# Optimization experiments

Measured on AMD Instinct MI355X. Metric: run time of the kernel, lower is better.

The kernel has to match this reference:

```python
import jax, jax.numpy as jnp
import numpy as np

C = 16  # CHANNELS
SOBEL_X = jnp.array([[-1., 0., 1.], [-2., 0., 2.], [-1., 0., 1.]], dtype=jnp.float32)
SOBEL_Y = SOBEL_X.T


def _depthwise3x3(x, k3):
    # x: [B,C,H,W]; k3: [3,3] kernel applied per-channel (groups=C, padding=1)
    k = jnp.broadcast_to(k3[None, None], (C, 1, 3, 3))
    return jax.lax.conv_general_dilated(x, k, window_strides=(1, 1), padding='SAME',
                                        feature_group_count=C)


def _alive_mask(x):
    # max_pool2d(alpha, k=3, s=1, p=1) > 0.1 on channel 3
    alpha = x[:, 3:4]
    pooled = jax.lax.reduce_window(alpha, -jnp.inf, jax.lax.max,
                                   (1, 1, 3, 3), (1, 1, 1, 1), 'SAME')
    return pooled > 0.1


def setup_inputs() -> dict:
    key = jax.random.key(0)
    k0, k1, k2, k3 = jax.random.split(key, 4)
    B = 1024
    state_grid = jax.random.uniform(k0, (B, C, 32, 32), dtype=jnp.float32)
    rand_mask = jax.random.randint(k1, (B, 1, 32, 32), 0, 2, dtype=jnp.int32)
    # dense_128: Conv2d(48, 128, k=1); torch default kaiming-uniform-ish -> use scaled normal
    w1 = jax.random.normal(k2, (128, 48), dtype=jnp.float32) * (1.0 / np.sqrt(48.0))
    b1 = jnp.zeros((128,), dtype=jnp.float32)
    # dense_16: original zero-init; use small random weights for a non-degenerate baseline
    w2 = jax.random.normal(k3, (16, 128), dtype=jnp.float32) * 0.01
    b2 = jnp.zeros((16,), dtype=jnp.float32)
    return {"state_grid": state_grid, "rand_mask": rand_mask,
            "w1": w1, "b1": b1, "w2": w2, "b2": b2}


def reference(state_grid, rand_mask, w1, b1, w2, b2):
    # perceive: depthwise sobel-x, sobel-y, identity -> concat to 48 channels
    px = _depthwise3x3(state_grid, SOBEL_X)
    py = _depthwise3x3(state_grid, SOBEL_Y)
    perception = jnp.concatenate([px, py, state_grid], axis=1)  # [B,48,32,32]
    # 1x1 conv MLP
    h = jax.nn.relu(jnp.einsum('oc,bchw->bohw', w1, perception) + b1[None, :, None, None])
    dx = jnp.einsum('oc,bchw->bohw', w2, h) + b2[None, :, None, None]  # [B,16,32,32]
    # stochastic update (0/1 mask broadcast over channels)
    x = state_grid + dx * rand_mask.astype(state_grid.dtype)
    # alive masking
    alive = _alive_mask(state_grid) & _alive_mask(x)
    x = x * alive.astype(state_grid.dtype)
    return jnp.clip(x, 0.0, 1.0)
```

## Files before the change

### kernel.cpp

```cpp
#include <hip/hip_runtime.h>
#include <hip/hip_bf16.h>

#define TPB 256

typedef __attribute__((ext_vector_type(8))) short short8v;
typedef __attribute__((ext_vector_type(4))) float f32x4;

__device__ __forceinline__ float bf2f(unsigned int u) {
    return __uint_as_float(u << 16);
}
__device__ __forceinline__ unsigned int packbf(float x, float y) {
    unsigned int r;
    asm("v_cvt_pk_bf16_f32 %0, %1, %2" : "=v"(r) : "v"(x), "v"(y));
    return r;
}
__device__ __forceinline__ short8v pack8(float4 a, float4 bq) {
    union { unsigned int u[4]; short8v s; } c;
    c.u[0] = packbf(a.x, a.y);  c.u[1] = packbf(a.z, a.w);
    c.u[2] = packbf(bq.x, bq.y); c.u[3] = packbf(bq.z, bq.w);
    return c.s;
}

__global__ __launch_bounds__(TPB, 2) void nca_mfma(
    const float* __restrict__ state,
    const int*   __restrict__ rmask,
    const float* __restrict__ w1,
    const float* __restrict__ b1,
    const float* __restrict__ w2,
    const float* __restrict__ b2,
    float* __restrict__ out)
{
    __shared__ __align__(16) unsigned short sSt[16 * 34 * 36];
    __shared__ __align__(16) unsigned short sP [64 * 72];
    __shared__ __align__(16) unsigned short sH [64 * 136];
    __shared__ __align__(16) float          sA [34 * 34];
    __shared__ unsigned char                sPre[1024];

    const int b    = blockIdx.x;
    const int tid  = threadIdx.x;
    const int lane = tid & 63;
    const int wv   = tid >> 6;
    const int lr   = lane & 15;
    const int lg   = lane >> 4;

    short8v w1f[8][2];
    short8v w2f[4];
    float   b1v[8];
    #pragma unroll
    for (int n = 0; n < 8; ++n) {
        const int f = lr * 8 + n;
        #pragma unroll
        for (int kk = 0; kk < 2; ++kk) {
            const int k0 = kk * 32 + lg * 8;
            if (k0 < 48) {
                const float4 x0 = *reinterpret_cast<const float4*>(w1 + f * 48 + k0);
                const float4 x1 = *reinterpret_cast<const float4*>(w1 + f * 48 + k0 + 4);
                w1f[n][kk] = pack8(x0, x1);
            } else {
                short8v z = {0,0,0,0,0,0,0,0};
                w1f[n][kk] = z;
            }
        }
        b1v[n] = b1[f];
    }
    #pragma unroll
    for (int ks = 0; ks < 4; ++ks) {
        const int k0 = ks * 32 + lg * 8;
        const float4 x0 = *reinterpret_cast<const float4*>(w2 + lr * 128 + k0);
        const float4 x1 = *reinterpret_cast<const float4*>(w2 + lr * 128 + k0 + 4);
        w2f[ks] = pack8(x0, x1);
    }
    const float b2v = b2[lr];

    for (int i = tid; i < 16*34*36/2; i += TPB) reinterpret_cast<unsigned int*>(sSt)[i] = 0u;
    for (int i = tid; i < 64*72/2;    i += TPB) reinterpret_cast<unsigned int*>(sP)[i]  = 0u;
    for (int i = tid; i < 34*34;      i += TPB) sA[i] = 0.f;
    __syncthreads();

    const float* gs = state + (size_t)b * 16384;
    #pragma unroll
    for (int k = 0; k < 16; ++k) {
        const int q = tid + k * TPB;
        const float4 v = reinterpret_cast<const float4*>(gs)[q];
        const int c = q >> 8, rem = q & 255;
        const int h = rem >> 3, wg = rem & 7;
        const int eo = c * 1224 + (h + 1) * 36 + (wg * 4 + 2);
        reinterpret_cast<unsigned int*>(&sSt[eo])[0] = packbf(v.x, v.y);
        reinterpret_cast<unsigned int*>(&sSt[eo])[1] = packbf(v.z, v.w);
    }
    __syncthreads();

    for (int p = tid; p < 1024; p += TPB) {
        const int h = p >> 5, w = p & 31;
        const unsigned short* sa = &sSt[3 * 1224 + h * 36 + (w + 1)];
        float m =          bf2f(sa[0]);
        m = fmaxf(m, bf2f(sa[1]));  m = fmaxf(m, bf2f(sa[2]));
        m = fmaxf(m, bf2f(sa[36])); m = fmaxf(m, bf2f(sa[37])); m = fmaxf(m, bf2f(sa[38]));
        m = fmaxf(m, bf2f(sa[72])); m = fmaxf(m, bf2f(sa[73])); m = fmaxf(m, bf2f(sa[74]));
        sPre[p] = (m > 0.1f) ? 1 : 0;
    }

    auto do_gate = [&](int pb, const float* xp) {
        float av = 0.f;
        if (lane < 16) {
            const int p = pb + lane;
            const int h = p >> 5, w = p & 31;
            const float* sa = &sA[h * 34 + w];
            float m =          sa[0];
            m = fmaxf(m, sa[1]);  m = fmaxf(m, sa[2]);
            m = fmaxf(m, sa[34]); m = fmaxf(m, sa[35]); m = fmaxf(m, sa[36]);
            m = fmaxf(m, sa[68]); m = fmaxf(m, sa[69]); m = fmaxf(m, sa[70]);
            av = ((m > 0.1f) && (sPre[p] != 0)) ? 1.f : 0.f;
        }
        const float g0 = __shfl(av, lg * 4 + 0);
        const float g1 = __shfl(av, lg * 4 + 1);
        const float g2 = __shfl(av, lg * 4 + 2);
        const float g3 = __shfl(av, lg * 4 + 3);
        float4 ov;
        ov.x = g0 * fminf(fmaxf(xp[0], 0.f), 1.f);
        ov.y = g1 * fminf(fmaxf(xp[1], 0.f), 1.f);
        ov.z = g2 * fminf(fmaxf(xp[2], 0.f), 1.f);
        ov.w = g3 * fminf(fmaxf(xp[3], 0.f), 1.f);
        *reinterpret_cast<float4*>(&out[(size_t)b * 16384 + lr * 1024 + pb + lg * 4]) = ov;
    };

    float xq[2][4];

    for (int s = 0; s < 16; ++s) {
        const int pbase = s * 64 + wv * 16;
        const int4   mi  = *reinterpret_cast<const int4*>(&rmask[b * 1024 + pbase + lg * 4]);
        const float4 idv = *reinterpret_cast<const float4*>(&state[(size_t)b * 16384 + lr * 1024 + pbase + lg * 4]);

        {
            const int cg   = lane & 7;
            const int pl   = lane >> 3;
            const int c0   = cg * 2;
            const int hloc = wv >> 1;
            const int w0   = (wv & 1) * 16 + pl * 2;
            const int h    = s * 2 + hloc;
            const int j0   = hloc * 32 + w0;
            float sx0[2], sx1[2], sy0[2], sy1[2], id0[2], id1[2];
            #pragma unroll
            for (int ci = 0; ci < 2; ++ci) {
                const unsigned short* bp = &sSt[(c0 + ci) * 1224 + h * 36 + w0];
                float A[3], Bv[3], Cv[3], D[3];
                #pragma unroll
                for (int dr = 0; dr < 3; ++dr) {
                    const unsigned int* rp = reinterpret_cast<const unsigned int*>(bp + dr * 36);
                    const unsigned int u0 = rp[0], u1 = rp[1], u2 = rp[2];
                    A[dr]  = bf2f(u0 >> 16);
                    Bv[dr] = bf2f(u1 & 0xffffu);
                    Cv[dr] = bf2f(u1 >> 16);
                    D[dr]  = bf2f(u2 & 0xffffu);
                }
                const float csa = A[0]  + 2.f * A[1]  + A[2];
                const float csb = Bv[0] + 2.f * Bv[1] + Bv[2];
                const float csc = Cv[0] + 2.f * Cv[1] + Cv[2];
                const float csd = D[0]  + 2.f * D[1]  + D[2];
                sx0[ci] = csc - csa;
                sx1[ci] = csd - csb;
                sy0[ci] = (A[2] + 2.f * Bv[2] + Cv[2]) - (A[0] + 2.f * Bv[0] + Cv[0]);
                sy1[ci] = (Bv[2] + 2.f * Cv[2] + D[2]) - (Bv[0] + 2.f * Cv[0] + D[0]);
                id0[ci] = Bv[1];
                id1[ci] = Cv[1];
            }
            unsigned int* r0 = reinterpret_cast<unsigned int*>(&sP[j0 * 72 + c0]);
            unsigned int* r1 = reinterpret_cast<unsigned int*>(&sP[(j0 + 1) * 72 + c0]);
            r0[0]  = packbf(sx0[0], sx0[1]);
            r0[8]  = packbf(sy0[0], sy0[1]);
            r0[16] = packbf(id0[0], id0[1]);
            r1[0]  = packbf(sx1[0], sx1[1]);
            r1[8]  = packbf(sy1[0], sy1[1]);
            r1[16] = packbf(id1[0], id1[1]);
        }

        f32x4 acc1[8];
        #pragma unroll
        for (int n = 0; n < 8; ++n) { acc1[n][0]=0.f; acc1[n][1]=0.f; acc1[n][2]=0.f; acc1[n][3]=0.f; }
        #pragma unroll
        for (int kk = 0; kk < 2; ++kk) {
            const short8v a = *reinterpret_cast<const short8v*>(&sP[(wv * 16 + lr) * 72 + kk * 32 + lg * 8]);
            #pragma unroll
            for (int n = 0; n < 8; ++n)
                acc1[n] = __builtin_amdgcn_mfma_f32_16x16x32_bf16(a, w1f[n][kk], acc1[n], 0, 0, 0);
        }
        #pragma unroll
        for (int r = 0; r < 4; ++r) {
            const int row = wv * 16 + lg * 4 + r;
            uint4 u;
            u.x = packbf(fmaxf(acc1[0][r] + b1v[0], 0.f), fmaxf(acc1[1][r] + b1v[1], 0.f));
            u.y = packbf(fmaxf(acc1[2][r] + b1v[2], 0.f), fmaxf(acc1[3][r] + b1v[3], 0.f));
            u.z = packbf(fmaxf(acc1[4][r] + b1v[4], 0.f), fmaxf(acc1[5][r] + b1v[5], 0.f));
            u.w = packbf(fmaxf(acc1[6][r] + b1v[6], 0.f), fmaxf(acc1[7][r] + b1v[7], 0.f));
            *reinterpret_cast<uint4*>(&sH[row * 136 + lr * 8]) = u;
        }

        f32x4 acc2; acc2[0]=0.f; acc2[1]=0.f; acc2[2]=0.f; acc2[3]=0.f;
        #pragma unroll
        for (int ksx = 0; ksx < 4; ++ksx) {
            const short8v a2 = *reinterpret_cast<const short8v*>(&sH[(wv * 16 + lr) * 136 + ksx * 32 + lg * 8]);
            acc2 = __builtin_amdgcn_mfma_f32_16x16x32_bf16(a2, w2f[ksx], acc2, 0, 0, 0);
        }
        float xv[4];
        xv[0] = fmaf(acc2[0] + b2v, (float)mi.x, idv.x);
        xv[1] = fmaf(acc2[1] + b2v, (float)mi.y, idv.y);
        xv[2] = fmaf(acc2[2] + b2v, (float)mi.z, idv.z);
        xv[3] = fmaf(acc2[3] + b2v, (float)mi.w, idv.w);
        if (lr == 3) {
            const int p0 = pbase + lg * 4;
            const int h2 = p0 >> 5, w2c = p0 & 31;
            float* dst = &sA[(h2 + 1) * 34 + (w2c + 1)];
            dst[0] = xv[0]; dst[1] = xv[1]; dst[2] = xv[2]; dst[3] = xv[3];
        }

        const int par = s & 1;
        if (s >= 2) do_gate((s - 2) * 64 + wv * 16, xq[par]);
        xq[par][0] = xv[0]; xq[par][1] = xv[1]; xq[par][2] = xv[2]; xq[par][3] = xv[3];

        __syncthreads();
    }
    do_gate(14 * 64 + wv * 16, xq[0]);
    do_gate(15 * 64 + wv * 16, xq[1]);
}

extern "C" void kernel_launch(void* const* d_in, const int* in_sizes, int n_in,
                              void* d_out, int out_size, void* d_ws, size_t ws_size,
                              hipStream_t stream) {
    const float* state = (const float*)d_in[0];
    const int*   rmask = (const int*)d_in[1];
    const float* w1    = (const float*)d_in[2];
    const float* b1    = (const float*)d_in[3];
    const float* w2    = (const float*)d_in[4];
    const float* b2    = (const float*)d_in[5];
    float* outp = (float*)d_out;

    const int B = in_sizes[0] / (16 * 32 * 32);
    hipLaunchKernelGGL(nca_mfma, dim3(B), dim3(TPB), 0, stream,
                       state, rmask, w1, b1, w2, b2, outp);
}
```

Baseline: 190.2 us.

## Stream state rows through ring buffer to cut LDS and raise occupancy

The full 34-row bf16 state halo tile in shared memory is replaced with an 8-row ring buffer. Each iteration prefetches the next rows from global memory and writes them in after compute, and the alive tile shrinks to a 9-row ring as well. The pre-update alive mask is now computed inline from the alpha channel during the Sobel stage instead of in a separate pass. Launch bounds go from 2 to 4 blocks per CU, so more blocks can be resident to hide latency, at the cost of tighter register budgets and more complex ring indexing.

```diff
diff --git a/kernel.cpp b/kernel.cpp
--- a/kernel.cpp
+++ b/kernel.cpp
@@ -21,7 +21,7 @@
     return c.s;
 }
 
-__global__ __launch_bounds__(TPB, 2) void nca_mfma(
+__global__ __launch_bounds__(TPB, 4) void nca_mfma(
     const float* __restrict__ state,
     const int*   __restrict__ rmask,
     const float* __restrict__ w1,
@@ -30,10 +30,10 @@
     const float* __restrict__ b2,
     float* __restrict__ out)
 {
-    __shared__ __align__(16) unsigned short sSt[16 * 34 * 36];
+    __shared__ __align__(16) unsigned short sSt[16 * 8 * 36];
     __shared__ __align__(16) unsigned short sP [64 * 72];
     __shared__ __align__(16) unsigned short sH [64 * 136];
-    __shared__ __align__(16) float          sA [34 * 34];
+    __shared__ __align__(16) float          sA [9 * 34];
     __shared__ unsigned char                sPre[1024];
 
     const int b    = blockIdx.x;
@@ -72,44 +72,41 @@
     }
     const float b2v = b2[lr];
 
-    for (int i = tid; i < 16*34*36/2; i += TPB) reinterpret_cast<unsigned int*>(sSt)[i] = 0u;
-    for (int i = tid; i < 64*72/2;    i += TPB) reinterpret_cast<unsigned int*>(sP)[i]  = 0u;
-    for (int i = tid; i < 34*34;      i += TPB) sA[i] = 0.f;
+    for (int i = tid; i < 16*8*36/2; i += TPB) reinterpret_cast<unsigned int*>(sSt)[i] = 0u;
+    for (int i = tid; i < 64*72/2;   i += TPB) reinterpret_cast<unsigned int*>(sP)[i]  = 0u;
+    for (int i = tid; i < 9*34;      i += TPB) sA[i] = 0.f;
     __syncthreads();
 
     const float* gs = state + (size_t)b * 16384;
     #pragma unroll
-    for (int k = 0; k < 16; ++k) {
+    for (int k = 0; k < 3; ++k) {
         const int q = tid + k * TPB;
-        const float4 v = reinterpret_cast<const float4*>(gs)[q];
-        const int c = q >> 8, rem = q & 255;
-        const int h = rem >> 3, wg = rem & 7;
-        const int eo = c * 1224 + (h + 1) * 36 + (wg * 4 + 2);
-        reinterpret_cast<unsigned int*>(&sSt[eo])[0] = packbf(v.x, v.y);
-        reinterpret_cast<unsigned int*>(&sSt[eo])[1] = packbf(v.z, v.w);
+        if (q < 640) {
+            const int ch = q / 40, rem = q - ch * 40;
+            const int row = rem >> 3, px4 = rem & 7;
+            const float4 v = reinterpret_cast<const float4*>(gs)[ch * 256 + row * 8 + px4];
+            unsigned int* dst = reinterpret_cast<unsigned int*>(&sSt[ch * 288 + row * 36 + px4 * 4 + 2]);
+            dst[0] = packbf(v.x, v.y);
+            dst[1] = packbf(v.z, v.w);
+        }
     }
     __syncthreads();
 
-    for (int p = tid; p < 1024; p += TPB) {
-        const int h = p >> 5, w = p & 31;
-        const unsigned short* sa = &sSt[3 * 1224 + h * 36 + (w + 1)];
-        float m =          bf2f(sa[0]);
-        m = fmaxf(m, bf2f(sa[1]));  m = fmaxf(m, bf2f(sa[2]));
-        m = fmaxf(m, bf2f(sa[36])); m = fmaxf(m, bf2f(sa[37])); m = fmaxf(m, bf2f(sa[38]));
-        m = fmaxf(m, bf2f(sa[72])); m = fmaxf(m, bf2f(sa[73])); m = fmaxf(m, bf2f(sa[74]));
-        sPre[p] = (m > 0.1f) ? 1 : 0;
-    }
-
-    auto do_gate = [&](int pb, const float* xp) {
+    auto do_gate = [&](int g, const float* xp) {
         float av = 0.f;
         if (lane < 16) {
-            const int p = pb + lane;
+            const int p = g * 64 + wv * 16 + lane;
             const int h = p >> 5, w = p & 31;
-            const float* sa = &sA[h * 34 + w];
-            float m =          sa[0];
-            m = fmaxf(m, sa[1]);  m = fmaxf(m, sa[2]);
-            m = fmaxf(m, sa[34]); m = fmaxf(m, sa[35]); m = fmaxf(m, sa[36]);
-            m = fmaxf(m, sa[68]); m = fmaxf(m, sa[69]); m = fmaxf(m, sa[70]);
+            const int sm = (h - 1 >= 0) ? ((h - 1) & 7) : 8;
+            const int s0 = h & 7;
+            const int sp = (h + 1 <= 31) ? ((h + 1) & 7) : 8;
+            const float* r0 = &sA[sm * 34 + w];
+            const float* r1 = &sA[s0 * 34 + w];
+            const float* r2 = &sA[sp * 34 + w];
+            float m =          r0[0];
+            m = fmaxf(m, r0[1]); m = fmaxf(m, r0[2]);
+            m = fmaxf(m, r1[0]); m = fmaxf(m, r1[1]); m = fmaxf(m, r1[2]);
+            m = fmaxf(m, r2[0]); m = fmaxf(m, r2[1]); m = fmaxf(m, r2[2]);
             av = ((m > 0.1f) && (sPre[p] != 0)) ? 1.f : 0.f;
         }
         const float g0 = __shfl(av, lg * 4 + 0);
@@ -121,15 +118,25 @@
         ov.y = g1 * fminf(fmaxf(xp[1], 0.f), 1.f);
         ov.z = g2 * fminf(fmaxf(xp[2], 0.f), 1.f);
         ov.w = g3 * fminf(fmaxf(xp[3], 0.f), 1.f);
-        *reinterpret_cast<float4*>(&out[(size_t)b * 16384 + lr * 1024 + pb + lg * 4]) = ov;
+        *reinterpret_cast<float4*>(&out[(size_t)b * 16384 + lr * 1024 + g * 64 + wv * 16 + lg * 4]) = ov;
     };
 
     float xq[2][4];
+
+    const int pf_ch  = tid >> 4;
+    const int pf_rl  = (tid & 15) >> 3;
+    const int pf_px4 = tid & 7;
 
     for (int s = 0; s < 16; ++s) {
         const int pbase = s * 64 + wv * 16;
         const int4   mi  = *reinterpret_cast<const int4*>(&rmask[b * 1024 + pbase + lg * 4]);
         const float4 idv = *reinterpret_cast<const float4*>(&state[(size_t)b * 16384 + lr * 1024 + pbase + lg * 4]);
+
+        const int pf_row = 2 * s + 5 + pf_rl;
+        float4 pf = {0.f, 0.f, 0.f, 0.f};
+        const bool pf_do = (pf_row <= 32);
+        if (pf_row <= 31)
+            pf = reinterpret_cast<const float4*>(gs)[pf_ch * 256 + pf_row * 8 + pf_px4];
 
         {
             const int cg   = lane & 7;
@@ -137,16 +144,18 @@
             const int c0   = cg * 2;
             const int hloc = wv >> 1;
             const int w0   = (wv & 1) * 16 + pl * 2;
-            const int h    = s * 2 + hloc;
+            const int rr0  = 2 * s + hloc - 1;
             const int j0   = hloc * 32 + w0;
             float sx0[2], sx1[2], sy0[2], sy1[2], id0[2], id1[2];
+            float mp0 = 0.f, mp1 = 0.f;
             #pragma unroll
             for (int ci = 0; ci < 2; ++ci) {
-                const unsigned short* bp = &sSt[(c0 + ci) * 1224 + h * 36 + w0];
+                const unsigned short* bp = &sSt[(c0 + ci) * 288 + w0];
                 float A[3], Bv[3], Cv[3], D[3];
                 #pragma unroll
                 for (int dr = 0; dr < 3; ++dr) {
-                    const unsigned int* rp = reinterpret_cast<const unsigned int*>(bp + dr * 36);
+                    const int slot = ((rr0 + dr) & 7) * 36;
+                    const unsigned int* rp = reinterpret_cast<const unsigned int*>(bp + slot);
                     const unsigned int u0 = rp[0], u1 = rp[1], u2 = rp[2];
                     A[dr]  = bf2f(u0 >> 16);
                     Bv[dr] = bf2f(u1 & 0xffffu);
@@ -163,6 +172,13 @@
                 sy1[ci] = (Bv[2] + 2.f * Cv[2] + D[2]) - (Bv[0] + 2.f * Cv[0] + D[0]);
                 id0[ci] = Bv[1];
                 id1[ci] = Cv[1];
+                if (ci == 1) {
+                    #pragma unroll
+                    for (int dr = 0; dr < 3; ++dr) {
+                        mp0 = fmaxf(mp0, fmaxf(fmaxf(A[dr], Bv[dr]), Cv[dr]));
+                        mp1 = fmaxf(mp1, fmaxf(fmaxf(Bv[dr], Cv[dr]), D[dr]));
+                    }
+                }
             }
             unsigned int* r0 = reinterpret_cast<unsigned int*>(&sP[j0 * 72 + c0]);
             unsigned int* r1 = reinterpret_cast<unsigned int*>(&sP[(j0 + 1) * 72 + c0]);
@@ -172,6 +188,10 @@
             r1[0]  = packbf(sx1[0], sx1[1]);
             r1[8]  = packbf(sy1[0], sy1[1]);
             r1[16] = packbf(id1[0], id1[1]);
+            if (cg == 1) {
+                sPre[s * 64 + j0]     = (mp0 > 0.1f) ? 1 : 0;
+                sPre[s * 64 + j0 + 1] = (mp1 > 0.1f) ? 1 : 0;
+            }
         }
 
         f32x4 acc1[8];
@@ -209,18 +229,25 @@
         if (lr == 3) {
             const int p0 = pbase + lg * 4;
             const int h2 = p0 >> 5, w2c = p0 & 31;
-            float* dst = &sA[(h2 + 1) * 34 + (w2c + 1)];
+            float* dst = &sA[(h2 & 7) * 34 + (w2c + 1)];
             dst[0] = xv[0]; dst[1] = xv[1]; dst[2] = xv[2]; dst[3] = xv[3];
         }
 
         const int par = s & 1;
-        if (s >= 2) do_gate((s - 2) * 64 + wv * 16, xq[par]);
+        if (s >= 2) do_gate(s - 2, xq[par]);
         xq[par][0] = xv[0]; xq[par][1] = xv[1]; xq[par][2] = xv[2]; xq[par][3] = xv[3];
 
+        if (pf_do) {
+            unsigned int* dst = reinterpret_cast<unsigned int*>(
+                &sSt[pf_ch * 288 + (pf_row & 7) * 36 + pf_px4 * 4 + 2]);
+            dst[0] = packbf(pf.x, pf.y);
+            dst[1] = packbf(pf.z, pf.w);
+        }
+
         __syncthreads();
     }
-    do_gate(14 * 64 + wv * 16, xq[0]);
-    do_gate(15 * 64 + wv * 16, xq[1]);
+    do_gate(14, xq[0]);
+    do_gate(15, xq[1]);
 }
 
 extern "C" void kernel_launch(void* const* d_in, const int* in_sizes, int n_in,
```

New measurement: 273.2 us. +43.6%, slower.

## Fold Sobel filters into first-layer weights and run perception as implicit-GEMM conv

Applied to the files above, without the earlier changes.

Premultiplies the w1 weights by the Sobel and identity taps so the 3x3 depthwise perception plus the first 1x1 layer become a single 3x3 convolution done by MFMA over a 144-wide K (9 taps x 16 channels, padded to 5 K-steps). The state is stored channel-last (HWC) in LDS so each MFMA A fragment is a direct 16-byte read of 8 channels at one tap. This removes the scalar Sobel stencil code and the sP staging buffer. In exchange it issues 40 MFMAs per step instead of 16, and it rounds the folded weights to bf16, which changes numerical behaviour slightly.

```diff
diff --git a/kernel.cpp b/kernel.cpp
--- a/kernel.cpp
+++ b/kernel.cpp
@@ -2,6 +2,7 @@
 #include <hip/hip_bf16.h>
 
 #define TPB 256
+#define RS  592
 
 typedef __attribute__((ext_vector_type(8))) short short8v;
 typedef __attribute__((ext_vector_type(4))) float f32x4;
@@ -13,6 +14,12 @@
     unsigned int r;
     asm("v_cvt_pk_bf16_f32 %0, %1, %2" : "=v"(r) : "v"(x), "v"(y));
     return r;
+}
+__device__ __forceinline__ short8v pack8f(const float* v) {
+    union { unsigned int u[4]; short8v s; } c;
+    c.u[0] = packbf(v[0], v[1]); c.u[1] = packbf(v[2], v[3]);
+    c.u[2] = packbf(v[4], v[5]); c.u[3] = packbf(v[6], v[7]);
+    return c.s;
 }
 __device__ __forceinline__ short8v pack8(float4 a, float4 bq) {
     union { unsigned int u[4]; short8v s; } c;
@@ -21,7 +28,7 @@
     return c.s;
 }
 
-__global__ __launch_bounds__(TPB, 2) void nca_mfma(
+__global__ __launch_bounds__(TPB, 2) void nca_conv(
     const float* __restrict__ state,
     const int*   __restrict__ rmask,
     const float* __restrict__ w1,
@@ -30,8 +37,7 @@
     const float* __restrict__ b2,
     float* __restrict__ out)
 {
-    __shared__ __align__(16) unsigned short sSt[16 * 34 * 36];
-    __shared__ __align__(16) unsigned short sP [64 * 72];
+    __shared__ __align__(16) unsigned short sSt[34 * RS];
     __shared__ __align__(16) unsigned short sH [64 * 136];
     __shared__ __align__(16) float          sA [34 * 34];
     __shared__ unsigned char                sPre[1024];
@@ -42,68 +48,101 @@
     const int wv   = tid >> 6;
     const int lr   = lane & 15;
     const int lg   = lane >> 4;
-
-    short8v w1f[8][2];
+    const int lh   = lg >> 1;
+    const int c0   = (lg & 1) * 8;
+
+
+    short8v w1f[8][5];
     short8v w2f[4];
     float   b1v[8];
-    #pragma unroll
-    for (int n = 0; n < 8; ++n) {
-        const int f = lr * 8 + n;
-        #pragma unroll
-        for (int kk = 0; kk < 2; ++kk) {
-            const int k0 = kk * 32 + lg * 8;
-            if (k0 < 48) {
-                const float4 x0 = *reinterpret_cast<const float4*>(w1 + f * 48 + k0);
-                const float4 x1 = *reinterpret_cast<const float4*>(w1 + f * 48 + k0 + 4);
-                w1f[n][kk] = pack8(x0, x1);
-            } else {
-                short8v z = {0,0,0,0,0,0,0,0};
-                w1f[n][kk] = z;
+    {
+        const float SXT[10] = {-1.f,0.f,1.f,-2.f,0.f,2.f,-1.f,0.f,1.f,0.f};
+        const float SYT[10] = {-1.f,-2.f,-1.f,0.f,0.f,0.f,1.f,2.f,1.f,0.f};
+        #pragma unroll
+        for (int n = 0; n < 8; ++n) {
+            const int f = lr * 8 + n;
+            float wx[8], wy[8], ws[8];
+            {
+                const float4 a0 = *reinterpret_cast<const float4*>(w1 + f*48 + c0);
+                const float4 a1 = *reinterpret_cast<const float4*>(w1 + f*48 + c0 + 4);
+                const float4 y0 = *reinterpret_cast<const float4*>(w1 + f*48 + 16 + c0);
+                const float4 y1 = *reinterpret_cast<const float4*>(w1 + f*48 + 16 + c0 + 4);
+                const float4 s0 = *reinterpret_cast<const float4*>(w1 + f*48 + 32 + c0);
+                const float4 s1 = *reinterpret_cast<const float4*>(w1 + f*48 + 32 + c0 + 4);
+                wx[0]=a0.x; wx[1]=a0.y; wx[2]=a0.z; wx[3]=a0.w; wx[4]=a1.x; wx[5]=a1.y; wx[6]=a1.z; wx[7]=a1.w;
+                wy[0]=y0.x; wy[1]=y0.y; wy[2]=y0.z; wy[3]=y0.w; wy[4]=y1.x; wy[5]=y1.y; wy[6]=y1.z; wy[7]=y1.w;
+                ws[0]=s0.x; ws[1]=s0.y; ws[2]=s0.z; ws[3]=s0.w; ws[4]=s1.x; ws[5]=s1.y; ws[6]=s1.z; ws[7]=s1.w;
             }
-        }
-        b1v[n] = b1[f];
-    }
-    #pragma unroll
-    for (int ks = 0; ks < 4; ++ks) {
-        const int k0 = ks * 32 + lg * 8;
-        const float4 x0 = *reinterpret_cast<const float4*>(w2 + lr * 128 + k0);
-        const float4 x1 = *reinterpret_cast<const float4*>(w2 + lr * 128 + k0 + 4);
-        w2f[ks] = pack8(x0, x1);
+            #pragma unroll
+            for (int kk = 0; kk < 5; ++kk) {
+                const float sx = lh ? SXT[2*kk+1] : SXT[2*kk];
+                const float sy = lh ? SYT[2*kk+1] : SYT[2*kk];
+                const float si = (kk == 2 && lh == 0) ? 1.f : 0.f;
+                const float kill = (kk == 4 && lh == 1) ? 0.f : 1.f;
+                float v[8];
+                #pragma unroll
+                for (int e = 0; e < 8; ++e)
+                    v[e] = (wx[e]*sx + wy[e]*sy + ws[e]*si) * kill;
+                w1f[n][kk] = pack8f(v);
+            }
+            b1v[n] = b1[f];
+        }
+        #pragma unroll
+        for (int ks = 0; ks < 4; ++ks) {
+            const int k0 = ks * 32 + lg * 8;
+            const float4 x0 = *reinterpret_cast<const float4*>(w2 + lr*128 + k0);
+            const float4 x1 = *reinterpret_cast<const float4*>(w2 + lr*128 + k0 + 4);
+            w2f[ks] = pack8(x0, x1);
+        }
     }
     const float b2v = b2[lr];
 
-    for (int i = tid; i < 16*34*36/2; i += TPB) reinterpret_cast<unsigned int*>(sSt)[i] = 0u;
-    for (int i = tid; i < 64*72/2;    i += TPB) reinterpret_cast<unsigned int*>(sP)[i]  = 0u;
-    for (int i = tid; i < 34*34;      i += TPB) sA[i] = 0.f;
+    for (int i = tid; i < 34*RS/2; i += TPB) reinterpret_cast<unsigned int*>(sSt)[i] = 0u;
+    for (int i = tid; i < 34*34;   i += TPB) sA[i] = 0.f;
     __syncthreads();
 
     const float* gs = state + (size_t)b * 16384;
     #pragma unroll
-    for (int k = 0; k < 16; ++k) {
-        const int q = tid + k * TPB;
-        const float4 v = reinterpret_cast<const float4*>(gs)[q];
-        const int c = q >> 8, rem = q & 255;
-        const int h = rem >> 3, wg = rem & 7;
-        const int eo = c * 1224 + (h + 1) * 36 + (wg * 4 + 2);
-        reinterpret_cast<unsigned int*>(&sSt[eo])[0] = packbf(v.x, v.y);
-        reinterpret_cast<unsigned int*>(&sSt[eo])[1] = packbf(v.z, v.w);
+    for (int i = 0; i < 8; ++i) {
+        const int q4 = tid + i * TPB;
+        const int cpair = q4 >> 8;
+        const int px4 = q4 & 255;
+        const int h = px4 >> 3, w4 = px4 & 7;
+        const float4 va = reinterpret_cast<const float4*>(gs)[cpair*512 + px4];
+        const float4 vb = reinterpret_cast<const float4*>(gs)[cpair*512 + 256 + px4];
+        unsigned int* dst = reinterpret_cast<unsigned int*>(sSt);
+        const int base = (h + 1) * (RS/2) + (w4*4 + 2) * 8 + cpair;
+        dst[base]      = packbf(va.x, vb.x);
+        dst[base + 8]  = packbf(va.y, vb.y);
+        dst[base + 16] = packbf(va.z, vb.z);
+        dst[base + 24] = packbf(va.w, vb.w);
     }
     __syncthreads();
 
     for (int p = tid; p < 1024; p += TPB) {
         const int h = p >> 5, w = p & 31;
-        const unsigned short* sa = &sSt[3 * 1224 + h * 36 + (w + 1)];
-        float m =          bf2f(sa[0]);
-        m = fmaxf(m, bf2f(sa[1]));  m = fmaxf(m, bf2f(sa[2]));
-        m = fmaxf(m, bf2f(sa[36])); m = fmaxf(m, bf2f(sa[37])); m = fmaxf(m, bf2f(sa[38]));
-        m = fmaxf(m, bf2f(sa[72])); m = fmaxf(m, bf2f(sa[73])); m = fmaxf(m, bf2f(sa[74]));
+        float m = 0.f;
+        #pragma unroll
+        for (int dr = 0; dr < 3; ++dr)
+            #pragma unroll
+            for (int dc = 0; dc < 3; ++dc)
+                m = fmaxf(m, bf2f(sSt[(h+dr)*RS + (w+1+dc)*16 + 3]));
         sPre[p] = (m > 0.1f) ? 1 : 0;
     }
 
-    auto do_gate = [&](int pb, const float* xp) {
+    int roff[5];
+    #pragma unroll
+    for (int kk = 0; kk < 5; ++kk) {
+        const int te = 2*kk, to = (2*kk+1 > 8) ? 8 : 2*kk+1;
+        const int re = (te/3)*RS + (te%3)*16;
+        const int ro = (to/3)*RS + (to%3)*16;
+        roff[kk] = lh ? ro : re;
+    }
+
+    auto do_gate = [&](int g, const float* xp) {
         float av = 0.f;
         if (lane < 16) {
-            const int p = pb + lane;
+            const int p = g * 64 + wv * 16 + lane;
             const int h = p >> 5, w = p & 31;
             const float* sa = &sA[h * 34 + w];
             float m =          sa[0];
@@ -121,7 +160,7 @@
         ov.y = g1 * fminf(fmaxf(xp[1], 0.f), 1.f);
         ov.z = g2 * fminf(fmaxf(xp[2], 0.f), 1.f);
         ov.w = g3 * fminf(fmaxf(xp[3], 0.f), 1.f);
-        *reinterpret_cast<float4*>(&out[(size_t)b * 16384 + lr * 1024 + pb + lg * 4]) = ov;
+        *reinterpret_cast<float4*>(&out[(size_t)b * 16384 + lr * 1024 + g * 64 + wv * 16 + lg * 4]) = ov;
     };
 
     float xq[2][4];
@@ -131,58 +170,24 @@
         const int4   mi  = *reinterpret_cast<const int4*>(&rmask[b * 1024 + pbase + lg * 4]);
         const float4 idv = *reinterpret_cast<const float4*>(&state[(size_t)b * 16384 + lr * 1024 + pbase + lg * 4]);
 
-        {
-            const int cg   = lane & 7;
-            const int pl   = lane >> 3;
-            const int c0   = cg * 2;
-            const int hloc = wv >> 1;
-            const int w0   = (wv & 1) * 16 + pl * 2;
-            const int h    = s * 2 + hloc;
-            const int j0   = hloc * 32 + w0;
-            float sx0[2], sx1[2], sy0[2], sy1[2], id0[2], id1[2];
-            #pragma unroll
-            for (int ci = 0; ci < 2; ++ci) {
-                const unsigned short* bp = &sSt[(c0 + ci) * 1224 + h * 36 + w0];
-                float A[3], Bv[3], Cv[3], D[3];
-                #pragma unroll
-                for (int dr = 0; dr < 3; ++dr) {
-                    const unsigned int* rp = reinterpret_cast<const unsigned int*>(bp + dr * 36);
-                    const unsigned int u0 = rp[0], u1 = rp[1], u2 = rp[2];
-                    A[dr]  = bf2f(u0 >> 16);
-                    Bv[dr] = bf2f(u1 & 0xffffu);
-                    Cv[dr] = bf2f(u1 >> 16);
-                    D[dr]  = bf2f(u2 & 0xffffu);
-                }
-                const float csa = A[0]  + 2.f * A[1]  + A[2];
-                const float csb = Bv[0] + 2.f * Bv[1] + Bv[2];
-                const float csc = Cv[0] + 2.f * Cv[1] + Cv[2];
-                const float csd = D[0]  + 2.f * D[1]  + D[2];
-                sx0[ci] = csc - csa;
-                sx1[ci] = csd - csb;
-                sy0[ci] = (A[2] + 2.f * Bv[2] + Cv[2]) - (A[0] + 2.f * Bv[0] + Cv[0]);
-                sy1[ci] = (Bv[2] + 2.f * Cv[2] + D[2]) - (Bv[0] + 2.f * Cv[0] + D[0]);
-                id0[ci] = Bv[1];
-                id1[ci] = Cv[1];
-            }
-            unsigned int* r0 = reinterpret_cast<unsigned int*>(&sP[j0 * 72 + c0]);
-            unsigned int* r1 = reinterpret_cast<unsigned int*>(&sP[(j0 + 1) * 72 + c0]);
-            r0[0]  = packbf(sx0[0], sx0[1]);
-            r0[8]  = packbf(sy0[0], sy0[1]);
-            r0[16] = packbf(id0[0], id0[1]);
-            r1[0]  = packbf(sx1[0], sx1[1]);
-            r1[8]  = packbf(sy1[0], sy1[1]);
-            r1[16] = packbf(id1[0], id1[1]);
-        }
+        const int p = pbase + lr;
+        const int h = p >> 5, w = p & 31;
+        const unsigned aBase = (unsigned)(h * RS + (w + 1) * 16 + c0);
+
+        short8v afr[5];
+        #pragma unroll
+        for (int kk = 0; kk < 5; ++kk)
+            afr[kk] = *reinterpret_cast<const short8v*>(&sSt[aBase + roff[kk]]);
+        if (lh) { short8v z = {0,0,0,0,0,0,0,0}; afr[4] = z; }
 
         f32x4 acc1[8];
         #pragma unroll
         for (int n = 0; n < 8; ++n) { acc1[n][0]=0.f; acc1[n][1]=0.f; acc1[n][2]=0.f; acc1[n][3]=0.f; }
         #pragma unroll
-        for (int kk = 0; kk < 2; ++kk) {
-            const short8v a = *reinterpret_cast<const short8v*>(&sP[(wv * 16 + lr) * 72 + kk * 32 + lg * 8]);
+        for (int kk = 0; kk < 5; ++kk) {
             #pragma unroll
             for (int n = 0; n < 8; ++n)
-                acc1[n] = __builtin_amdgcn_mfma_f32_16x16x32_bf16(a, w1f[n][kk], acc1[n], 0, 0, 0);
+                acc1[n] = __builtin_amdgcn_mfma_f32_16x16x32_bf16(afr[kk], w1f[n][kk], acc1[n], 0, 0, 0);
         }
         #pragma unroll
         for (int r = 0; r < 4; ++r) {
@@ -214,13 +219,13 @@
         }
 
         const int par = s & 1;
-        if (s >= 2) do_gate((s - 2) * 64 + wv * 16, xq[par]);
+        if (s >= 2) do_gate(s - 2, xq[par]);
         xq[par][0] = xv[0]; xq[par][1] = xv[1]; xq[par][2] = xv[2]; xq[par][3] = xv[3];
 
         __syncthreads();
     }
-    do_gate(14 * 64 + wv * 16, xq[0]);
-    do_gate(15 * 64 + wv * 16, xq[1]);
+    do_gate(14, xq[0]);
+    do_gate(15, xq[1]);
 }
 
 extern "C" void kernel_launch(void* const* d_in, const int* in_sizes, int n_in,
@@ -235,6 +240,6 @@
     float* outp = (float*)d_out;
 
     const int B = in_sizes[0] / (16 * 32 * 32);
-    hipLaunchKernelGGL(nca_mfma, dim3(B), dim3(TPB), 0, stream,
+    hipLaunchKernelGGL(nca_conv, dim3(B), dim3(TPB), 0, stream,
                        state, rmask, w1, b1, w2, b2, outp);
 }
```

New measurement: 211.4 us. 1.11x slower.

## Split alive-mask gating into a separate kernel to drop per-step block barriers

Applied to the files above, without the earlier changes.

Moves the pre/post alive-mask max-pool, clamp and gating out of the fused MLP kernel into a second kernel. The first kernel now writes the ungated update straight to the output and no longer needs the shared alpha buffer, the delayed two-step gating pipeline or the per-iteration __syncthreads. The goal is to free the MLP loop from block-wide synchronisation and extra shared-memory work. In exchange the output is written, read back and rewritten, a slice of the state is read again, and a second kernel launch is added.

```diff
diff --git a/kernel.cpp b/kernel.cpp
--- a/kernel.cpp
+++ b/kernel.cpp
@@ -21,7 +21,7 @@
     return c.s;
 }
 
-__global__ __launch_bounds__(TPB, 2) void nca_mfma(
+__global__ __launch_bounds__(TPB, 2) void nca_mlp(
     const float* __restrict__ state,
     const int*   __restrict__ rmask,
     const float* __restrict__ w1,
@@ -33,8 +33,6 @@
     __shared__ __align__(16) unsigned short sSt[16 * 34 * 36];
     __shared__ __align__(16) unsigned short sP [64 * 72];
     __shared__ __align__(16) unsigned short sH [64 * 136];
-    __shared__ __align__(16) float          sA [34 * 34];
-    __shared__ unsigned char                sPre[1024];
 
     const int b    = blockIdx.x;
     const int tid  = threadIdx.x;
@@ -74,7 +72,6 @@
 
     for (int i = tid; i < 16*34*36/2; i += TPB) reinterpret_cast<unsigned int*>(sSt)[i] = 0u;
     for (int i = tid; i < 64*72/2;    i += TPB) reinterpret_cast<unsigned int*>(sP)[i]  = 0u;
-    for (int i = tid; i < 34*34;      i += TPB) sA[i] = 0.f;
     __syncthreads();
 
     const float* gs = state + (size_t)b * 16384;
@@ -90,55 +87,19 @@
     }
     __syncthreads();
 
-    for (int p = tid; p < 1024; p += TPB) {
-        const int h = p >> 5, w = p & 31;
-        const unsigned short* sa = &sSt[3 * 1224 + h * 36 + (w + 1)];
-        float m =          bf2f(sa[0]);
-        m = fmaxf(m, bf2f(sa[1]));  m = fmaxf(m, bf2f(sa[2]));
-        m = fmaxf(m, bf2f(sa[36])); m = fmaxf(m, bf2f(sa[37])); m = fmaxf(m, bf2f(sa[38]));
-        m = fmaxf(m, bf2f(sa[72])); m = fmaxf(m, bf2f(sa[73])); m = fmaxf(m, bf2f(sa[74]));
-        sPre[p] = (m > 0.1f) ? 1 : 0;
-    }
-
-    auto do_gate = [&](int pb, const float* xp) {
-        float av = 0.f;
-        if (lane < 16) {
-            const int p = pb + lane;
-            const int h = p >> 5, w = p & 31;
-            const float* sa = &sA[h * 34 + w];
-            float m =          sa[0];
-            m = fmaxf(m, sa[1]);  m = fmaxf(m, sa[2]);
-            m = fmaxf(m, sa[34]); m = fmaxf(m, sa[35]); m = fmaxf(m, sa[36]);
-            m = fmaxf(m, sa[68]); m = fmaxf(m, sa[69]); m = fmaxf(m, sa[70]);
-            av = ((m > 0.1f) && (sPre[p] != 0)) ? 1.f : 0.f;
-        }
-        const float g0 = __shfl(av, lg * 4 + 0);
-        const float g1 = __shfl(av, lg * 4 + 1);
-        const float g2 = __shfl(av, lg * 4 + 2);
-        const float g3 = __shfl(av, lg * 4 + 3);
-        float4 ov;
-        ov.x = g0 * fminf(fmaxf(xp[0], 0.f), 1.f);
-        ov.y = g1 * fminf(fmaxf(xp[1], 0.f), 1.f);
-        ov.z = g2 * fminf(fmaxf(xp[2], 0.f), 1.f);
-        ov.w = g3 * fminf(fmaxf(xp[3], 0.f), 1.f);
-        *reinterpret_cast<float4*>(&out[(size_t)b * 16384 + lr * 1024 + pb + lg * 4]) = ov;
-    };
-
-    float xq[2][4];
-
     for (int s = 0; s < 16; ++s) {
         const int pbase = s * 64 + wv * 16;
         const int4   mi  = *reinterpret_cast<const int4*>(&rmask[b * 1024 + pbase + lg * 4]);
         const float4 idv = *reinterpret_cast<const float4*>(&state[(size_t)b * 16384 + lr * 1024 + pbase + lg * 4]);
 
         {
-            const int cg   = lane & 7;
-            const int pl   = lane >> 3;
-            const int c0   = cg * 2;
-            const int hloc = wv >> 1;
-            const int w0   = (wv & 1) * 16 + pl * 2;
-            const int h    = s * 2 + hloc;
-            const int j0   = hloc * 32 + w0;
+            const int cg = tid & 7;
+            const int pp = tid >> 3;
+            const int c0 = cg * 2;
+            const int hloc = pp >> 4;
+            const int h  = s * 2 + hloc;
+            const int w0 = (pp & 15) * 2;
+            const int j0 = hloc * 32 + w0;
             float sx0[2], sx1[2], sy0[2], sy1[2], id0[2], id1[2];
             #pragma unroll
             for (int ci = 0; ci < 2; ++ci) {
@@ -201,26 +162,65 @@
             const short8v a2 = *reinterpret_cast<const short8v*>(&sH[(wv * 16 + lr) * 136 + ksx * 32 + lg * 8]);
             acc2 = __builtin_amdgcn_mfma_f32_16x16x32_bf16(a2, w2f[ksx], acc2, 0, 0, 0);
         }
-        float xv[4];
-        xv[0] = fmaf(acc2[0] + b2v, (float)mi.x, idv.x);
-        xv[1] = fmaf(acc2[1] + b2v, (float)mi.y, idv.y);
-        xv[2] = fmaf(acc2[2] + b2v, (float)mi.z, idv.z);
-        xv[3] = fmaf(acc2[3] + b2v, (float)mi.w, idv.w);
-        if (lr == 3) {
-            const int p0 = pbase + lg * 4;
-            const int h2 = p0 >> 5, w2c = p0 & 31;
-            float* dst = &sA[(h2 + 1) * 34 + (w2c + 1)];
-            dst[0] = xv[0]; dst[1] = xv[1]; dst[2] = xv[2]; dst[3] = xv[3];
-        }
-
-        const int par = s & 1;
-        if (s >= 2) do_gate((s - 2) * 64 + wv * 16, xq[par]);
-        xq[par][0] = xv[0]; xq[par][1] = xv[1]; xq[par][2] = xv[2]; xq[par][3] = xv[3];
-
-        __syncthreads();
-    }
-    do_gate(14 * 64 + wv * 16, xq[0]);
-    do_gate(15 * 64 + wv * 16, xq[1]);
+        float4 ov;
+        ov.x = fmaf(acc2[0] + b2v, (float)mi.x, idv.x);
+        ov.y = fmaf(acc2[1] + b2v, (float)mi.y, idv.y);
+        ov.z = fmaf(acc2[2] + b2v, (float)mi.z, idv.z);
+        ov.w = fmaf(acc2[3] + b2v, (float)mi.w, idv.w);
+        *reinterpret_cast<float4*>(&out[(size_t)b * 16384 + lr * 1024 + pbase + lg * 4]) = ov;
+    }
+}
+
+__global__ __launch_bounds__(256) void nca_gate(
+    const float* __restrict__ state,
+    float* __restrict__ out)
+{
+    __shared__ float aPre [34 * 34];
+    __shared__ float aPost[34 * 34];
+    const int b = blockIdx.x, t = threadIdx.x;
+
+    for (int i = t; i < 34 * 34; i += 256) { aPre[i] = 0.f; aPost[i] = 0.f; }
+    __syncthreads();
+
+    const int h  = t >> 3;
+    const int w4 = (t & 7) * 4;
+    {
+        const float4 sv = reinterpret_cast<const float4*>(state + (size_t)b * 16384 + 3072)[t];
+        const float4 xv = reinterpret_cast<const float4*>(out   + (size_t)b * 16384 + 3072)[t];
+        float* dp = &aPre [(h + 1) * 34 + w4 + 1];
+        float* dq = &aPost[(h + 1) * 34 + w4 + 1];
+        dp[0] = sv.x; dp[1] = sv.y; dp[2] = sv.z; dp[3] = sv.w;
+        dq[0] = xv.x; dq[1] = xv.y; dq[2] = xv.z; dq[3] = xv.w;
+    }
+    __syncthreads();
+
+    float g[4];
+    #pragma unroll
+    for (int k = 0; k < 4; ++k) {
+        const int base = h * 34 + w4 + k;
+        const float* p = &aPre[base];
+        const float* q = &aPost[base];
+        float m1 = p[0];
+        m1 = fmaxf(m1, p[1]);  m1 = fmaxf(m1, p[2]);
+        m1 = fmaxf(m1, p[34]); m1 = fmaxf(m1, p[35]); m1 = fmaxf(m1, p[36]);
+        m1 = fmaxf(m1, p[68]); m1 = fmaxf(m1, p[69]); m1 = fmaxf(m1, p[70]);
+        float m2 = q[0];
+        m2 = fmaxf(m2, q[1]);  m2 = fmaxf(m2, q[2]);
+        m2 = fmaxf(m2, q[34]); m2 = fmaxf(m2, q[35]); m2 = fmaxf(m2, q[36]);
+        m2 = fmaxf(m2, q[68]); m2 = fmaxf(m2, q[69]); m2 = fmaxf(m2, q[70]);
+        g[k] = ((m1 > 0.1f) && (m2 > 0.1f)) ? 1.f : 0.f;
+    }
+
+    float* ob = out + (size_t)b * 16384;
+    #pragma unroll
+    for (int c = 0; c < 16; ++c) {
+        float4 v = reinterpret_cast<const float4*>(ob + c * 1024)[t];
+        v.x = g[0] * fminf(fmaxf(v.x, 0.f), 1.f);
+        v.y = g[1] * fminf(fmaxf(v.y, 0.f), 1.f);
+        v.z = g[2] * fminf(fmaxf(v.z, 0.f), 1.f);
+        v.w = g[3] * fminf(fmaxf(v.w, 0.f), 1.f);
+        reinterpret_cast<float4*>(ob + c * 1024)[t] = v;
+    }
 }
 
 extern "C" void kernel_launch(void* const* d_in, const int* in_sizes, int n_in,
@@ -235,6 +235,8 @@
     float* outp = (float*)d_out;
 
     const int B = in_sizes[0] / (16 * 32 * 32);
-    hipLaunchKernelGGL(nca_mfma, dim3(B), dim3(TPB), 0, stream,
+    hipLaunchKernelGGL(nca_mlp,  dim3(B), dim3(TPB), 0, stream,
                        state, rmask, w1, b1, w2, b2, outp);
-}
+    hipLaunchKernelGGL(nca_gate, dim3(B), dim3(256), 0, stream,
+                       state, outp);
+}
```

After: 184.2 us. 3.1% less time.
